# Performance work log

Hardware: AMD Instinct MI355X
Metric: run time of the kernel (lower is better)

## Reference

```python
import jax, jax.numpy as jnp
import numpy as np

IN, H, OUT = 28, 64, 10


def _rnn_layer(x_proj, W_hh):
    # x_proj: [T, B, H] time-major, already x @ W_ih^T + b_ih + b_hh
    B = x_proj.shape[1]
    h0 = jnp.zeros((B, H), dtype=x_proj.dtype)

    def step(h, xt):
        h = jnp.tanh(xt + h @ W_hh.T)
        return h, h

    _, hs = jax.lax.scan(step, h0, x_proj)
    return hs  # [T, B, H]


def setup_inputs() -> dict:
    key = jax.random.key(0)
    ks = jax.random.split(key, 12)
    s = 1.0 / np.sqrt(H)  # PyTorch RNN init scale
    B, T = 4096, 256
    return {
        "x": jax.random.normal(ks[0], (B, T, IN), dtype=jnp.float32),
        "W_ih0": jax.random.uniform(ks[1], (H, IN), minval=-s, maxval=s),
        "W_hh0": jax.random.uniform(ks[2], (H, H), minval=-s, maxval=s),
        "b_ih0": jax.random.uniform(ks[3], (H,), minval=-s, maxval=s),
        "b_hh0": jax.random.uniform(ks[4], (H,), minval=-s, maxval=s),
        "W_ih1": jax.random.uniform(ks[5], (H, H), minval=-s, maxval=s),
        "W_hh1": jax.random.uniform(ks[6], (H, H), minval=-s, maxval=s),
        "b_ih1": jax.random.uniform(ks[7], (H,), minval=-s, maxval=s),
        "b_hh1": jax.random.uniform(ks[8], (H,), minval=-s, maxval=s),
        "W_fc": jax.random.uniform(ks[9], (OUT, H), minval=-s, maxval=s),
        "b_fc": jax.random.uniform(ks[10], (OUT,), minval=-s, maxval=s),
    }


def reference(x, W_ih0, W_hh0, b_ih0, b_hh0, W_ih1, W_hh1, b_ih1, b_hh1, W_fc, b_fc):
    # Layer 0: batch input projection as one big GEMM, then sequential scan
    xt = jnp.swapaxes(x, 0, 1)                      # [T, B, IN]
    p0 = xt @ W_ih0.T + (b_ih0 + b_hh0)             # [T, B, H]
    h0_seq = _rnn_layer(p0, W_hh0)                  # [T, B, H]
    # Layer 1
    p1 = h0_seq @ W_ih1.T + (b_ih1 + b_hh1)         # [T, B, H]
    h1_seq = _rnn_layer(p1, W_hh1)                  # [T, B, H]
    # fc on last timestep
    return h1_seq[-1] @ W_fc.T + b_fc               # [B, OUT]
```

## Files before the change

kernel.cpp:

```cpp
#include <hip/hip_runtime.h>

#define TT   256
#define INH  28
#define HH   64
#define OUTN 10

__device__ __forceinline__ float fast_tanh(float x) {
    float cx = fminf(fmaxf(x, -15.0f), 15.0f);
    float e2 = __expf(2.0f * cx);
    return 1.0f - 2.0f * __builtin_amdgcn_rcpf(e2 + 1.0f);
}

__global__ __launch_bounds__(256, 2)
void rnn2_fused(const float* __restrict__ x,
                const float* __restrict__ Wih0, const float* __restrict__ Whh0,
                const float* __restrict__ bih0, const float* __restrict__ bhh0,
                const float* __restrict__ Wih1, const float* __restrict__ Whh1,
                const float* __restrict__ bih1, const float* __restrict__ bhh1,
                const float* __restrict__ Wfc,  const float* __restrict__ bfc,
                float* __restrict__ out)
{
    __shared__ float h0s[8][HH];
    __shared__ float h1s[8][HH];

    const int tid  = threadIdx.x;
    const int lane = tid & 63;
    const int wave = __builtin_amdgcn_readfirstlane(tid >> 6);

    float wih0[INH];
#pragma unroll
    for (int k = 0; k < INH; ++k) wih0[k] = Wih0[lane * INH + k];
    float whh0[HH];
#pragma unroll
    for (int k = 0; k < HH; ++k) whh0[k] = Whh0[lane * HH + k];
    float wih1[HH];
#pragma unroll
    for (int k = 0; k < HH; ++k) wih1[k] = Wih1[lane * HH + k];
    float whh1[HH];
#pragma unroll
    for (int k = 0; k < HH; ++k) whh1[k] = Whh1[lane * HH + k];

    const float bias0 = bih0[lane] + bhh0[lane];
    const float bias1 = bih1[lane] + bhh1[lane];

    const int slot0 = wave * 2 + 0;
    const int slot1 = wave * 2 + 1;
    const int b0 = __builtin_amdgcn_readfirstlane((int)blockIdx.x * 8 + wave * 2);
    const int b1 = b0 + 1;

    h0s[slot0][lane] = 0.0f; h0s[slot1][lane] = 0.0f;
    h1s[slot0][lane] = 0.0f; h1s[slot1][lane] = 0.0f;

    const float4* xq0 = (const float4*)(x + (size_t)b0 * (TT * INH));
    const float4* xq1 = (const float4*)(x + (size_t)b1 * (TT * INH));

    const float4* h0q0 = (const float4*)h0s[slot0];
    const float4* h0q1 = (const float4*)h0s[slot1];
    const float4* h1q0 = (const float4*)h1s[slot0];
    const float4* h1q1 = (const float4*)h1s[slot1];

#pragma unroll 1
    for (int t = 0; t < TT; ++t) {
        const float4* xr0 = xq0 + t * 7;
        const float4* xr1 = xq1 + t * 7;

        float pa0 = bias0, pb0 = 0.0f, pa1 = bias0, pb1 = 0.0f;
#pragma unroll
        for (int i = 0; i < 7; ++i) {
            float4 a = xr0[i], b = xr1[i];
            pa0 = fmaf(a.x, wih0[4*i+0], pa0); pa1 = fmaf(b.x, wih0[4*i+0], pa1);
            pb0 = fmaf(a.y, wih0[4*i+1], pb0); pb1 = fmaf(b.y, wih0[4*i+1], pb1);
            pa0 = fmaf(a.z, wih0[4*i+2], pa0); pa1 = fmaf(b.z, wih0[4*i+2], pa1);
            pb0 = fmaf(a.w, wih0[4*i+3], pb0); pb1 = fmaf(b.w, wih0[4*i+3], pb1);
        }
#pragma unroll
        for (int kk = 0; kk < 16; ++kk) {
            float4 a = h0q0[kk], b = h0q1[kk];
            pa0 = fmaf(a.x, whh0[4*kk+0], pa0); pa1 = fmaf(b.x, whh0[4*kk+0], pa1);
            pb0 = fmaf(a.y, whh0[4*kk+1], pb0); pb1 = fmaf(b.y, whh0[4*kk+1], pb1);
            pa0 = fmaf(a.z, whh0[4*kk+2], pa0); pa1 = fmaf(b.z, whh0[4*kk+2], pa1);
            pb0 = fmaf(a.w, whh0[4*kk+3], pb0); pb1 = fmaf(b.w, whh0[4*kk+3], pb1);
        }
        float nh00 = fast_tanh(pa0 + pb0);
        float nh01 = fast_tanh(pa1 + pb1);
        h0s[slot0][lane] = nh00;
        h0s[slot1][lane] = nh01;

        float qa0 = bias1, qb0 = 0.0f, qa1 = bias1, qb1 = 0.0f;
#pragma unroll
        for (int kk = 0; kk < 16; ++kk) {
            float4 a = h0q0[kk], b = h0q1[kk];
            qa0 = fmaf(a.x, wih1[4*kk+0], qa0); qa1 = fmaf(b.x, wih1[4*kk+0], qa1);
            qb0 = fmaf(a.y, wih1[4*kk+1], qb0); qb1 = fmaf(b.y, wih1[4*kk+1], qb1);
            qa0 = fmaf(a.z, wih1[4*kk+2], qa0); qa1 = fmaf(b.z, wih1[4*kk+2], qa1);
            qb0 = fmaf(a.w, wih1[4*kk+3], qb0); qb1 = fmaf(b.w, wih1[4*kk+3], qb1);
        }
#pragma unroll
        for (int kk = 0; kk < 16; ++kk) {
            float4 c = h1q0[kk], d = h1q1[kk];
            qa0 = fmaf(c.x, whh1[4*kk+0], qa0); qa1 = fmaf(d.x, whh1[4*kk+0], qa1);
            qb0 = fmaf(c.y, whh1[4*kk+1], qb0); qb1 = fmaf(d.y, whh1[4*kk+1], qb1);
            qa0 = fmaf(c.z, whh1[4*kk+2], qa0); qa1 = fmaf(d.z, whh1[4*kk+2], qa1);
            qb0 = fmaf(c.w, whh1[4*kk+3], qb0); qb1 = fmaf(d.w, whh1[4*kk+3], qb1);
        }
        float nh10 = fast_tanh(qa0 + qb0);
        float nh11 = fast_tanh(qa1 + qb1);
        h1s[slot0][lane] = nh10;
        h1s[slot1][lane] = nh11;
    }

    if (lane < OUTN) {
        const float4* wrow = (const float4*)(Wfc + lane * HH);
        float acc0 = bfc[lane];
        float acc1 = acc0;
#pragma unroll
        for (int kk = 0; kk < 16; ++kk) {
            float4 w = wrow[kk];
            float4 a = h1q0[kk], b = h1q1[kk];
            acc0 = fmaf(a.x, w.x, acc0); acc1 = fmaf(b.x, w.x, acc1);
            acc0 = fmaf(a.y, w.y, acc0); acc1 = fmaf(b.y, w.y, acc1);
            acc0 = fmaf(a.z, w.z, acc0); acc1 = fmaf(b.z, w.z, acc1);
            acc0 = fmaf(a.w, w.w, acc0); acc1 = fmaf(b.w, w.w, acc1);
        }
        out[(size_t)b0 * OUTN + lane] = acc0;
        out[(size_t)b1 * OUTN + lane] = acc1;
    }
}

extern "C" void kernel_launch(void* const* d_in, const int* in_sizes, int n_in,
                              void* d_out, int out_size, void* d_ws, size_t ws_size,
                              hipStream_t stream) {
    const float* x    = (const float*)d_in[0];
    const float* Wih0 = (const float*)d_in[1];
    const float* Whh0 = (const float*)d_in[2];
    const float* bih0 = (const float*)d_in[3];
    const float* bhh0 = (const float*)d_in[4];
    const float* Wih1 = (const float*)d_in[5];
    const float* Whh1 = (const float*)d_in[6];
    const float* bih1 = (const float*)d_in[7];
    const float* bhh1 = (const float*)d_in[8];
    const float* Wfc  = (const float*)d_in[9];
    const float* bfc  = (const float*)d_in[10];
    float* out = (float*)d_out;

    rnn2_fused<<<512, 256, 0, stream>>>(x, Wih0, Whh0, bih0, bhh0,
                                        Wih1, Whh1, bih1, bhh1, Wfc, bfc, out);
}
```

Baseline: 783.8 us.

## Split batch between fused single-wave kernel and layer-pipelined two-wave kernel

Runs the fused kernel as one wave per block over the first half of the batch. A new kernel handles the second half, with one wave per layer: layer 0 writes its hidden state into a double-buffered LDS ring that layer 1 reads one step behind, so the two recurrences overlap. Both kernels stage each timestep's x through LDS with a one-step-ahead prefetch, replacing the earlier direct float4 global reads in the inner loop. This trades a __syncthreads every step and two launches on the same stream for more parallelism per batch pair.

```diff
diff --git a/kernel.cpp b/kernel.cpp
--- a/kernel.cpp
+++ b/kernel.cpp
@@ -11,21 +11,23 @@
     return 1.0f - 2.0f * __builtin_amdgcn_rcpf(e2 + 1.0f);
 }
 
-__global__ __launch_bounds__(256, 2)
+__global__ __launch_bounds__(64)
+__attribute__((amdgpu_waves_per_eu(2, 2)))
 void rnn2_fused(const float* __restrict__ x,
                 const float* __restrict__ Wih0, const float* __restrict__ Whh0,
                 const float* __restrict__ bih0, const float* __restrict__ bhh0,
                 const float* __restrict__ Wih1, const float* __restrict__ Whh1,
                 const float* __restrict__ bih1, const float* __restrict__ bhh1,
                 const float* __restrict__ Wfc,  const float* __restrict__ bfc,
-                float* __restrict__ out)
+                float* __restrict__ out, int row0)
 {
-    __shared__ float h0s[8][HH];
-    __shared__ float h1s[8][HH];
-
-    const int tid  = threadIdx.x;
-    const int lane = tid & 63;
-    const int wave = __builtin_amdgcn_readfirstlane(tid >> 6);
+    __shared__ __align__(16) float h0s[2][HH];
+    __shared__ __align__(16) float h1s[2][HH];
+    __shared__ __align__(16) float xl[2][64];
+
+    const int lane = threadIdx.x;
+    const int b0 = row0 + (int)blockIdx.x * 2;
+    const int b1 = b0 + 1;
 
     float wih0[INH];
 #pragma unroll
@@ -43,31 +45,30 @@
     const float bias0 = bih0[lane] + bhh0[lane];
     const float bias1 = bih1[lane] + bhh1[lane];
 
-    const int slot0 = wave * 2 + 0;
-    const int slot1 = wave * 2 + 1;
-    const int b0 = __builtin_amdgcn_readfirstlane((int)blockIdx.x * 8 + wave * 2);
-    const int b1 = b0 + 1;
-
-    h0s[slot0][lane] = 0.0f; h0s[slot1][lane] = 0.0f;
-    h1s[slot0][lane] = 0.0f; h1s[slot1][lane] = 0.0f;
-
-    const float4* xq0 = (const float4*)(x + (size_t)b0 * (TT * INH));
-    const float4* xq1 = (const float4*)(x + (size_t)b1 * (TT * INH));
-
-    const float4* h0q0 = (const float4*)h0s[slot0];
-    const float4* h0q1 = (const float4*)h0s[slot1];
-    const float4* h1q0 = (const float4*)h1s[slot0];
-    const float4* h1q1 = (const float4*)h1s[slot1];
+    int xrow = (lane < INH) ? b0 : b1;
+    int xcol = (lane < INH) ? lane : (lane - INH);
+    if (lane >= 2 * INH) { xrow = b1; xcol = INH - 1; }
+    const float* xbase = x + (size_t)xrow * (TT * INH) + xcol;
+
+    h0s[0][lane] = 0.0f; h0s[1][lane] = 0.0f;
+    h1s[0][lane] = 0.0f; h1s[1][lane] = 0.0f;
+    xl[0][lane] = xbase[0];
+
+    const float4* h0q0 = (const float4*)h0s[0];
+    const float4* h0q1 = (const float4*)h0s[1];
+    const float4* h1q0 = (const float4*)h1s[0];
+    const float4* h1q1 = (const float4*)h1s[1];
 
 #pragma unroll 1
     for (int t = 0; t < TT; ++t) {
-        const float4* xr0 = xq0 + t * 7;
-        const float4* xr1 = xq1 + t * 7;
+        const int tn = (t + 1 < TT) ? (t + 1) : (TT - 1);
+        const float xv = xbase[(size_t)tn * INH];
+        const float4* xq = (const float4*)xl[t & 1];
 
         float pa0 = bias0, pb0 = 0.0f, pa1 = bias0, pb1 = 0.0f;
 #pragma unroll
         for (int i = 0; i < 7; ++i) {
-            float4 a = xr0[i], b = xr1[i];
+            float4 a = xq[i], b = xq[7 + i];
             pa0 = fmaf(a.x, wih0[4*i+0], pa0); pa1 = fmaf(b.x, wih0[4*i+0], pa1);
             pb0 = fmaf(a.y, wih0[4*i+1], pb0); pb1 = fmaf(b.y, wih0[4*i+1], pb1);
             pa0 = fmaf(a.z, wih0[4*i+2], pa0); pa1 = fmaf(b.z, wih0[4*i+2], pa1);
@@ -81,12 +82,20 @@
             pa0 = fmaf(a.z, whh0[4*kk+2], pa0); pa1 = fmaf(b.z, whh0[4*kk+2], pa1);
             pb0 = fmaf(a.w, whh0[4*kk+3], pb0); pb1 = fmaf(b.w, whh0[4*kk+3], pb1);
         }
-        float nh00 = fast_tanh(pa0 + pb0);
-        float nh01 = fast_tanh(pa1 + pb1);
-        h0s[slot0][lane] = nh00;
-        h0s[slot1][lane] = nh01;
+        const float nh00 = fast_tanh(pa0 + pb0);
+        const float nh01 = fast_tanh(pa1 + pb1);
+        h0s[0][lane] = nh00;
+        h0s[1][lane] = nh01;
 
         float qa0 = bias1, qb0 = 0.0f, qa1 = bias1, qb1 = 0.0f;
+#pragma unroll
+        for (int kk = 0; kk < 16; ++kk) {
+            float4 c = h1q0[kk], d = h1q1[kk];
+            qa0 = fmaf(c.x, whh1[4*kk+0], qa0); qa1 = fmaf(d.x, whh1[4*kk+0], qa1);
+            qb0 = fmaf(c.y, whh1[4*kk+1], qb0); qb1 = fmaf(d.y, whh1[4*kk+1], qb1);
+            qa0 = fmaf(c.z, whh1[4*kk+2], qa0); qa1 = fmaf(d.z, whh1[4*kk+2], qa1);
+            qb0 = fmaf(c.w, whh1[4*kk+3], qb0); qb1 = fmaf(d.w, whh1[4*kk+3], qb1);
+        }
 #pragma unroll
         for (int kk = 0; kk < 16; ++kk) {
             float4 a = h0q0[kk], b = h0q1[kk];
@@ -95,21 +104,150 @@
             qa0 = fmaf(a.z, wih1[4*kk+2], qa0); qa1 = fmaf(b.z, wih1[4*kk+2], qa1);
             qb0 = fmaf(a.w, wih1[4*kk+3], qb0); qb1 = fmaf(b.w, wih1[4*kk+3], qb1);
         }
-#pragma unroll
-        for (int kk = 0; kk < 16; ++kk) {
-            float4 c = h1q0[kk], d = h1q1[kk];
-            qa0 = fmaf(c.x, whh1[4*kk+0], qa0); qa1 = fmaf(d.x, whh1[4*kk+0], qa1);
-            qb0 = fmaf(c.y, whh1[4*kk+1], qb0); qb1 = fmaf(d.y, whh1[4*kk+1], qb1);
-            qa0 = fmaf(c.z, whh1[4*kk+2], qa0); qa1 = fmaf(d.z, whh1[4*kk+2], qa1);
-            qb0 = fmaf(c.w, whh1[4*kk+3], qb0); qb1 = fmaf(d.w, whh1[4*kk+3], qb1);
-        }
-        float nh10 = fast_tanh(qa0 + qb0);
-        float nh11 = fast_tanh(qa1 + qb1);
-        h1s[slot0][lane] = nh10;
-        h1s[slot1][lane] = nh11;
+        h1s[0][lane] = fast_tanh(qa0 + qb0);
+        h1s[1][lane] = fast_tanh(qa1 + qb1);
+
+        xl[(t + 1) & 1][lane] = xv;
     }
 
     if (lane < OUTN) {
+        const float4* wrow = (const float4*)(Wfc + lane * HH);
+        float acc0 = bfc[lane];
+        float acc1 = acc0;
+#pragma unroll
+        for (int kk = 0; kk < 16; ++kk) {
+            float4 w = wrow[kk];
+            float4 a = h1q0[kk], b = h1q1[kk];
+            acc0 = fmaf(a.x, w.x, acc0); acc1 = fmaf(b.x, w.x, acc1);
+            acc0 = fmaf(a.y, w.y, acc0); acc1 = fmaf(b.y, w.y, acc1);
+            acc0 = fmaf(a.z, w.z, acc0); acc1 = fmaf(b.z, w.z, acc1);
+            acc0 = fmaf(a.w, w.w, acc0); acc1 = fmaf(b.w, w.w, acc1);
+        }
+        out[(size_t)b0 * OUTN + lane] = acc0;
+        out[(size_t)b1 * OUTN + lane] = acc1;
+    }
+}
+
+__global__ __launch_bounds__(128)
+__attribute__((amdgpu_waves_per_eu(2, 2)))
+void rnn2_split(const float* __restrict__ x,
+                const float* __restrict__ Wih0, const float* __restrict__ Whh0,
+                const float* __restrict__ bih0, const float* __restrict__ bhh0,
+                const float* __restrict__ Wih1, const float* __restrict__ Whh1,
+                const float* __restrict__ bih1, const float* __restrict__ bhh1,
+                const float* __restrict__ Wfc,  const float* __restrict__ bfc,
+                float* __restrict__ out, int row0)
+{
+    __shared__ __align__(16) float ring[2][2][HH];
+    __shared__ __align__(16) float h1s[2][HH];
+    __shared__ __align__(16) float xl[2][64];
+
+    const int tid  = threadIdx.x;
+    const int lane = tid & 63;
+    const int wave = tid >> 6;
+    const int b0 = row0 + (int)blockIdx.x * 2;
+    const int b1 = b0 + 1;
+
+    float wA[HH], wB[HH];
+    float bias;
+    if (wave == 0) {
+#pragma unroll
+        for (int k = 0; k < HH; ++k) wA[k] = Whh0[lane * HH + k];
+#pragma unroll
+        for (int k = 0; k < INH; ++k) wB[k] = Wih0[lane * INH + k];
+#pragma unroll
+        for (int k = INH; k < HH; ++k) wB[k] = 0.0f;
+        bias = bih0[lane] + bhh0[lane];
+    } else {
+#pragma unroll
+        for (int k = 0; k < HH; ++k) wA[k] = Whh1[lane * HH + k];
+#pragma unroll
+        for (int k = 0; k < HH; ++k) wB[k] = Wih1[lane * HH + k];
+        bias = bih1[lane] + bhh1[lane];
+    }
+
+    int xrow = (lane < INH) ? b0 : b1;
+    int xcol = (lane < INH) ? lane : (lane - INH);
+    if (lane >= 2 * INH) { xrow = b1; xcol = INH - 1; }
+    const float* xbase = x + (size_t)xrow * (TT * INH) + xcol;
+
+    if (wave == 0) {
+        ring[0][0][lane] = 0.0f; ring[0][1][lane] = 0.0f;
+        ring[1][0][lane] = 0.0f; ring[1][1][lane] = 0.0f;
+        xl[0][lane] = xbase[0];
+    } else {
+        h1s[0][lane] = 0.0f; h1s[1][lane] = 0.0f;
+    }
+    __syncthreads();
+
+    float nh00 = 0.0f, nh01 = 0.0f;
+
+    const float4* h1q0 = (const float4*)h1s[0];
+    const float4* h1q1 = (const float4*)h1s[1];
+
+#pragma unroll 1
+    for (int t = 0; t <= TT + 1; ++t) {
+        if (wave == 0) {
+            if (t >= 1 && t <= TT) {
+                ring[(t - 1) & 1][0][lane] = nh00;
+                ring[(t - 1) & 1][1][lane] = nh01;
+            }
+            if (t < TT) {
+                const int tn = (t + 1 < TT) ? (t + 1) : (TT - 1);
+                const float xv = xbase[(size_t)tn * INH];
+                const float4* xq = (const float4*)xl[t & 1];
+                const float4* s0 = (const float4*)ring[(t + 1) & 1][0];
+                const float4* s1 = (const float4*)ring[(t + 1) & 1][1];
+                float pa0 = bias, pb0 = 0.0f, pa1 = bias, pb1 = 0.0f;
+#pragma unroll
+                for (int i = 0; i < 7; ++i) {
+                    float4 a = xq[i], b = xq[7 + i];
+                    pa0 = fmaf(a.x, wB[4*i+0], pa0); pa1 = fmaf(b.x, wB[4*i+0], pa1);
+                    pb0 = fmaf(a.y, wB[4*i+1], pb0); pb1 = fmaf(b.y, wB[4*i+1], pb1);
+                    pa0 = fmaf(a.z, wB[4*i+2], pa0); pa1 = fmaf(b.z, wB[4*i+2], pa1);
+                    pb0 = fmaf(a.w, wB[4*i+3], pb0); pb1 = fmaf(b.w, wB[4*i+3], pb1);
+                }
+#pragma unroll
+                for (int kk = 0; kk < 16; ++kk) {
+                    float4 a = s0[kk], b = s1[kk];
+                    pa0 = fmaf(a.x, wA[4*kk+0], pa0); pa1 = fmaf(b.x, wA[4*kk+0], pa1);
+                    pb0 = fmaf(a.y, wA[4*kk+1], pb0); pb1 = fmaf(b.y, wA[4*kk+1], pb1);
+                    pa0 = fmaf(a.z, wA[4*kk+2], pa0); pa1 = fmaf(b.z, wA[4*kk+2], pa1);
+                    pb0 = fmaf(a.w, wA[4*kk+3], pb0); pb1 = fmaf(b.w, wA[4*kk+3], pb1);
+                }
+                nh00 = fast_tanh(pa0 + pb0);
+                nh01 = fast_tanh(pa1 + pb1);
+                xl[(t + 1) & 1][lane] = xv;
+            }
+        } else {
+            if (t >= 2) {
+                const float4* s0 = (const float4*)ring[t & 1][0];
+                const float4* s1 = (const float4*)ring[t & 1][1];
+                float qa0 = bias, qb0 = 0.0f, qa1 = bias, qb1 = 0.0f;
+#pragma unroll
+                for (int kk = 0; kk < 16; ++kk) {
+                    float4 a = s0[kk], b = s1[kk];
+                    qa0 = fmaf(a.x, wB[4*kk+0], qa0); qa1 = fmaf(b.x, wB[4*kk+0], qa1);
+                    qb0 = fmaf(a.y, wB[4*kk+1], qb0); qb1 = fmaf(b.y, wB[4*kk+1], qb1);
+                    qa0 = fmaf(a.z, wB[4*kk+2], qa0); qa1 = fmaf(b.z, wB[4*kk+2], qa1);
+                    qb0 = fmaf(a.w, wB[4*kk+3], qb0); qb1 = fmaf(b.w, wB[4*kk+3], qb1);
+                }
+#pragma unroll
+                for (int kk = 0; kk < 16; ++kk) {
+                    float4 c = h1q0[kk], d = h1q1[kk];
+                    qa0 = fmaf(c.x, wA[4*kk+0], qa0); qa1 = fmaf(d.x, wA[4*kk+0], qa1);
+                    qb0 = fmaf(c.y, wA[4*kk+1], qb0); qb1 = fmaf(d.y, wA[4*kk+1], qb1);
+                    qa0 = fmaf(c.z, wA[4*kk+2], qa0); qa1 = fmaf(d.z, wA[4*kk+2], qa1);
+                    qb0 = fmaf(c.w, wA[4*kk+3], qb0); qb1 = fmaf(d.w, wA[4*kk+3], qb1);
+                }
+                h1s[0][lane] = fast_tanh(qa0 + qb0);
+                h1s[1][lane] = fast_tanh(qa1 + qb1);
+            }
+        }
+        __syncthreads();
+    }
+
+    if (wave == 1 && lane < OUTN) {
         const float4* wrow = (const float4*)(Wfc + lane * HH);
         float acc0 = bfc[lane];
         float acc1 = acc0;
@@ -143,6 +281,8 @@
     const float* bfc  = (const float*)d_in[10];
     float* out = (float*)d_out;
 
-    rnn2_fused<<<512, 256, 0, stream>>>(x, Wih0, Whh0, bih0, bhh0,
-                                        Wih1, Whh1, bih1, bhh1, Wfc, bfc, out);
-}
+    rnn2_fused<<<1024, 64, 0, stream>>>(x, Wih0, Whh0, bih0, bhh0,
+                                        Wih1, Whh1, bih1, bhh1, Wfc, bfc, out, 0);
+    rnn2_split<<<1024, 128, 0, stream>>>(x, Wih0, Whh0, bih0, bhh0,
+                                         Wih1, Whh1, bih1, bhh1, Wfc, bfc, out, 2048);
+}
```

Measured after the change: 1.314 ms. 1.68x slower.
